# Performance work log

Hardware: AMD Instinct MI355X
Metric: run time of the kernel (lower is better)

The kernel has to match this reference:

```python
import jax, jax.numpy as jnp
import numpy as np

LP = 512   # paragraph length (sequential steps)
LQ = 512   # question/context length attended over
B = 24     # batch_size global in source
IN = 150   # in_size (encoder output dim)
H = 150    # self.hidden_size = 2*75


def setup_inputs() -> dict:
    key = jax.random.key(0)
    ks = jax.random.split(key, 12)
    sc = 1.0 / np.sqrt(2 * IN)  # keep pre-activations in a sane range
    return {
        "up": jax.random.normal(ks[0], (LP, B, IN), jnp.float32),
        "uq": jax.random.normal(ks[1], (LQ, B, IN), jnp.float32),
        "v0": jax.random.normal(ks[2], (B, H), jnp.float32),
        "V": jax.random.normal(ks[3], (B, H, 1), jnp.float32),
        "Wp": jax.random.normal(ks[4], (H, 2 * IN), jnp.float32) * sc,
        "Wq": jax.random.normal(ks[5], (H, 2 * IN), jnp.float32) * sc,
        "Wv": jax.random.normal(ks[6], (H, H), jnp.float32) * sc,
        "Wg": jax.random.normal(ks[7], (4 * IN, 4 * IN), jnp.float32) * sc,
        "w_ih": jax.random.normal(ks[8], (3 * H, 2 * IN), jnp.float32) * sc,
        "w_hh": jax.random.normal(ks[9], (3 * H, H), jnp.float32) * sc,
        "b_ih": jnp.zeros((3 * H,), jnp.float32),
        "b_hh": jnp.zeros((3 * H,), jnp.float32),
    }


def _gru_cell(x, h, w_ih, w_hh, b_ih, b_hh):
    # torch.nn.GRUCell semantics
    gi = x @ w_ih.T + b_ih            # [B, 3H]
    gh = h @ w_hh.T + b_hh            # [B, 3H]
    i_r, i_z, i_n = jnp.split(gi, 3, axis=1)
    h_r, h_z, h_n = jnp.split(gh, 3, axis=1)
    r = jax.nn.sigmoid(i_r + h_r)
    z = jax.nn.sigmoid(i_z + h_z)
    n = jnp.tanh(i_n + r * h_n)
    return (1.0 - z) * n + z * h


def reference(up, uq, v0, V, Wp, Wq, Wv, Wg, w_ih, w_hh, b_ih, b_hh):
    in_size = up.shape[-1]
    # mixer = arange -> up[mixer] == up, so concat duplicates features
    Up = jnp.concatenate([up, up], axis=-1)   # [lp, B, 2*in]
    Uq = jnp.concatenate([uq, uq], axis=-1)   # [lq, B, 2*in]
    WUq = jnp.einsum('lbd,hd->lbh', Uq, Wq)   # loop-invariant Wq(Uq), [lq,B,H]
    Uq_b = Uq.transpose(1, 0, 2)              # [B, lq, 2*in]
    Vv = V[:, :, 0]                            # [B, H]

    def step(v, Up_i):                         # Up_i: [B, 2*in]
        Wup = Up_i @ Wp.T                      # [B, H]
        Wvv = v @ Wv.T                         # [B, H]
        x = jnp.tanh(WUq + Wup[None] + Wvv[None])      # [lq, B, H]
        s = jnp.einsum('lbh,bh->bl', x, Vv)            # [B, lq]
        a = jax.nn.softmax(s, axis=1)                  # [B, lq]
        c = jnp.einsum('bl,bld->bd', a, Uq_b)          # [B, 2*in]
        r = jnp.concatenate([Up_i, c], axis=1)         # [B, 4*in]
        g = jax.nn.sigmoid(r @ Wg.T)                   # [B, 4*in]
        c_ = (g * r)[:, 2 * in_size:]                  # gated attended vector
        v_new = _gru_cell(c_, v, w_ih, w_hh, b_ih, b_hh)
        return v_new, v_new

    _, vs = jax.lax.scan(step, v0, Up)  # [lp, B, H]
    # nn.Dropout in eval mode = identity
    return vs
```

## Files before the change

kernel.cpp:

```cpp
#include <hip/hip_runtime.h>
#include <hip/hip_fp16.h>

typedef _Float16 h2 __attribute__((ext_vector_type(2)));

#define OFF_EW     0u
#define OFF_UQT    983040u
#define OFF_WAV    1904640u
#define OFF_WGC    1952640u
#define OFF_WIH    1976640u
#define OFF_WQST   2048640u
#define OFF_WPC    2071140u
#define OFF_WGU    2093940u
#define OFF_UPA    2139540u
#define OFF_GU     3982740u
#define OFF_FLAG   7669140u
#define OFF_EXG    7669156u
#define OFF_XFLG   7709092u
#define WS_FLOATS  7709476u

__device__ __forceinline__ float fast_rcp(float x) { return __builtin_amdgcn_rcpf(x); }
__device__ __forceinline__ float fast_tanh(float x) {
  return 1.f - 2.f * fast_rcp(__expf(2.f * x) + 1.f);
}
__device__ __forceinline__ float fast_sigmoid(float x) {
  return fast_rcp(1.f + __expf(-x));
}

#if defined(__has_builtin)
#if __has_builtin(__builtin_amdgcn_fdot2)
#define HAVE_FDOT2 1
#endif
#if __has_builtin(__builtin_amdgcn_s_setprio)
#define HAVE_SETPRIO 1
#endif
#endif

__device__ __forceinline__ float fdot2(h2 a, h2 b, float c) {
#ifdef HAVE_FDOT2
  return __builtin_amdgcn_fdot2(a, b, c, false);
#else
  return c + (float)a[0] * (float)b[0] + (float)a[1] * (float)b[1];
#endif
}

__device__ __forceinline__ void ast(float* p, float v) {
  __hip_atomic_store(p, v, __ATOMIC_RELAXED, __HIP_MEMORY_SCOPE_AGENT);
}
__device__ __forceinline__ float ald(const float* p) {
  return __hip_atomic_load(p, __ATOMIC_RELAXED, __HIP_MEMORY_SCOPE_AGENT);
}

__global__ void prep_weights(const float* __restrict__ Wq, const float* __restrict__ Wp,
                             const float* __restrict__ Wv, const float* __restrict__ Wg,
                             const float* __restrict__ w_ih, const float* __restrict__ w_hh,
                             float* __restrict__ ws) {
  float* wqsT = ws + OFF_WQST;
  float* WPC  = ws + OFF_WPC;
  float* WGU  = ws + OFF_WGU;
  _Float16* WAV = (_Float16*)(ws + OFF_WAV);
  _Float16* WGC = (_Float16*)(ws + OFF_WGC);
  _Float16* WIHh = (_Float16*)(ws + OFF_WIH);

  int idx = blockIdx.x * blockDim.x + threadIdx.x;
  int n = gridDim.x * blockDim.x;

  for (int i = idx; i < 150 * 150; i += n) {
    int d = i / 150, h = i - d * 150;
    wqsT[i] = Wq[h * 300 + d] + Wq[h * 300 + d + 150];
  }
  for (int i = idx; i < 600 * 160; i += n) {
    int r = i / 160, h = i - r * 160;
    float v = 0.f;
    if (h < 150) v = (r < 150) ? 2.f * Wv[r * 150 + h] : w_hh[(r - 150) * 150 + h];
    WAV[i] = (_Float16)v;
  }
  for (int i = idx; i < 300 * 160; i += n) {
    int r = i / 160, h = i - r * 160;
    int row = (300 + r) * 600;
    float v = (h < 150) ? Wg[row + 300 + h] + Wg[row + 450 + h] : 0.f;
    WGC[i] = (_Float16)v;
  }
  for (int i = idx; i < 450 * 320; i += n) {
    int r = i / 320, p = i - r * 320;
    float v = (p < 300) ? w_ih[r * 300 + p] : 0.f;
    WIHh[i] = (_Float16)v;
  }
  for (int i = idx; i < 150 * 152; i += n) {
    int h = i / 152, d = i - h * 152;
    WPC[i] = (d < 150) ? 2.f * (Wp[h * 300 + d] + Wp[h * 300 + 150 + d]) : 0.f;
  }
  for (int i = idx; i < 300 * 152; i += n) {
    int r = i / 152, d = i - r * 152;
    int row = (300 + r) * 600;
    WGU[i] = (d < 150) ? Wg[row + d] + Wg[row + 150 + d] : 0.f;
  }
  {
    unsigned* xf = (unsigned*)(ws + OFF_XFLG);
    for (int i = idx; i < 24 * 16; i += n) xf[i] = 0u;
  }
}

__global__ __launch_bounds__(192) void prep_ew(const float* __restrict__ uq, float* __restrict__ ws) {
  const float* wqsT = ws + OFF_WQST;
  _Float16* EW = (_Float16*)(ws + OFF_EW);
  const int l = blockIdx.x, b = blockIdx.y;
  __shared__ float sx[150], sDot[150];
  const int t = threadIdx.x;
  if (t < 150) sx[t] = uq[((size_t)l * 24 + b) * 150 + t];
  __syncthreads();
  if (t < 150) {
    float acc = 0.f;
    for (int d = 0; d < 150; ++d) acc += sx[d] * wqsT[d * 150 + t];
    sDot[t] = acc;
  }
  __syncthreads();
  if (t < 160) {
    float val = 1.f;
    if (t < 150) {
      val = __expf(2.f * sDot[t]);
      val = fminf(fmaxf(val, 1e-7f), 60000.f);
    }
    EW[((size_t)b * 512 + l) * 160 + t] = (_Float16)val;
  }
}

__global__ void prep_uqt(const float* __restrict__ uq, float* __restrict__ ws) {
  _Float16* UQT = (_Float16*)(ws + OFF_UQT);
  int idx = blockIdx.x * blockDim.x + threadIdx.x;
  int n = gridDim.x * blockDim.x;
  for (int m = idx; m < 24 * 150 * 512; m += n) {
    int b = m / (150 * 512);
    int rem = m - b * 150 * 512;
    int r = rem >> 9;
    int l = rem & 511;
    UQT[m] = (_Float16)uq[((size_t)l * 24 + b) * 150 + r];
  }
}

__global__ __launch_bounds__(256) void prep_upagu(const float* __restrict__ up, float* __restrict__ ws) {
  const int b = blockIdx.x;
  const int it = blockIdx.y;
  __shared__ float sUp[64][153];
  for (int m = threadIdx.x; m < 64 * 150; m += 256) {
    int il = m / 150, d = m - il * 150;
    sUp[il][d] = up[(((size_t)(it * 64 + il)) * 24 + b) * 150 + d];
  }
  __syncthreads();
  const float* WGU = ws + OFF_WGU;
  const float* WPC = ws + OFF_WPC;
  float* GU  = ws + OFF_GU  + ((size_t)b * 512 + it * 64) * 300;
  float* UPA = ws + OFF_UPA + ((size_t)b * 512 + it * 64) * 150;
  const int il = threadIdx.x & 63, rl = threadIdx.x >> 6;
  for (int r = rl; r < 450; r += 4) {
    const float* w = (r < 300) ? (WGU + (size_t)r * 152) : (WPC + (size_t)(r - 300) * 152);
    float acc = 0.f;
    for (int d = 0; d < 150; ++d) acc = fmaf(w[d], sUp[il][d], acc);
    if (r < 300) GU[(size_t)il * 300 + r] = acc;
    else         UPA[(size_t)il * 150 + (r - 300)] = acc;
  }
}

__global__ __launch_bounds__(1024) void pq_main(
    const float* __restrict__ v0, const float* __restrict__ Vfull,
    const float* __restrict__ b_ih, const float* __restrict__ b_hh,
    float* __restrict__ ws, float* __restrict__ out) {
  const int blk = blockIdx.x;
  const int x = blk & 7, s = blk >> 3;
  int t3 = -1;
  if (s == 0 || s == 1) t3 = 0;
  else if (s == 10 || s == 11) t3 = 1;
  else if (s == 20 || s == 21) t3 = 2;

  if (t3 < 0) {
    if (threadIdx.x >= 64) return;
    unsigned* flag = (unsigned*)(ws + OFF_FLAG);
    const unsigned long long start = __builtin_amdgcn_s_memrealtime();
    float a0 = 0.f, a1 = 0.f, a2 = 0.f, a3 = 0.f, a4 = 0.f, a5 = 0.f, a6 = 0.f, a7 = 0.f;
    const float m = 1.0000001f, c = 0.9999999f;
    for (;;) {
      #pragma unroll 32
      for (int k = 0; k < 1024; ++k) {
        a0 = fmaf(a0, m, c); a1 = fmaf(a1, m, c); a2 = fmaf(a2, m, c); a3 = fmaf(a3, m, c);
        a4 = fmaf(a4, m, c); a5 = fmaf(a5, m, c); a6 = fmaf(a6, m, c); a7 = fmaf(a7, m, c);
      }
      if (__hip_atomic_load(flag, __ATOMIC_RELAXED, __HIP_MEMORY_SCOPE_AGENT) == 0xDEADBEEFu) break;
      if (__builtin_amdgcn_s_memrealtime() - start > 3000000ull) break;
    }
    float sink = ((a0 + a1) + (a2 + a3)) + ((a4 + a5) + (a6 + a7));
    if (sink == 123.456789f) out[0] = sink;
    return;
  }

#ifdef HAVE_SETPRIO
  __builtin_amdgcn_s_setprio(3);
#endif

  const int hf = s & 1;
  const int b = x + 8 * t3;
  const int tid = threadIdx.x;

  const int EYB = hf ? 80 : 0, EYW = hf ? 70 : 80;
  const int PEYB = hf ? 0 : 80, PEYW = hf ? 80 : 70;
  const int CQB = hf ? 160 : 0, CQW = hf ? 140 : 160;
  const int NA  = 4 * EYW;
  const int NP4 = 3 * EYW;

  const _Float16* EWh  = (const _Float16*)(ws + OFF_EW);
  const _Float16* UQTh = (const _Float16*)(ws + OFF_UQT);
  const _Float16* WAV  = (const _Float16*)(ws + OFF_WAV);
  const _Float16* WIHh = (const _Float16*)(ws + OFF_WIH);
  const float* UPAb = ws + OFF_UPA + (size_t)b * 512 * 150;
  const float* GUb  = ws + OFF_GU  + (size_t)b * 512 * 300;

  float* EX = ws + OFF_EXG + (size_t)b * 1664;
  float* exS0 = EX;
  float* exS1 = EX + 512;
  float* exC  = EX + 1024;
  float* exCQ = EX + 1184;
  float* exV  = EX + 1488;
  float* exSmine = hf ? exS1 : exS0;
  unsigned* FLG = (unsigned*)(ws + OFF_XFLG);
  unsigned* myflag = FLG + (b * 16 + hf * 8);
  unsigned* pflag  = FLG + (b * 16 + (1 - hf) * 8);

  __shared__ float sTmpA[608];
  __shared__ float eyl[160];
  __shared__ float vvl[160];
  __shared__ float sC[152];
  __shared__ float sGip[456];
  __shared__ float sBih[456], sBhh[456];
  __shared__ float sVl[152];
  __shared__ float sRed[8], sRedB[8];
  __shared__ float sSumV;
  __shared__ h2 sAhp2[272];
  __shared__ h2 vop2[80];
  __shared__ h2 ox2[80];
  __shared__ h2 cq2[160];
  __shared__ h2 sWv2[12000];
  __shared__ h2 sWGC2[24000];
  _Float16* sAhx = (_Float16*)sAhp2;
  _Float16* vop = (_Float16*)vop2;
  _Float16* ox  = (_Float16*)ox2;
  _Float16* cq  = (_Float16*)cq2;

  const int g = tid >> 3, j = tid & 7;
  const int g16 = tid >> 4, j16 = tid & 15;

  if (tid < 160) {
    vop[tid] = (_Float16)((tid < 150) ? v0[b * 150 + tid] : 0.f);
    vvl[tid] = (tid < 150) ? Vfull[b * 150 + tid] : 0.f;
    eyl[tid] = 1.f;
  } else if (tid < 320) {
    ox[tid - 160] = (_Float16)0.f;
  } else if (tid < 640) {
    cq[tid - 320] = (_Float16)0.f;
  }
  if (tid >= 512 && tid < 968) {
    int p = tid - 512;
    sBih[p] = (p < 450) ? b_ih[p] : 0.f;
    sBhh[p] = (p < 450) ? b_hh[p] : 0.f;
  }
  if (tid < 152) sVl[tid] = (tid < 150) ? v0[b * 150 + tid] : 0.f;
  {
    const unsigned* srcv = (const unsigned*)(ws + OFF_WAV);
    unsigned* dv = (unsigned*)sWv2;
    for (int k = tid; k < 12000; k += 1024) dv[k] = srcv[k];
    const unsigned* srcg = (const unsigned*)(ws + OFF_WGC);
    unsigned* dg = (unsigned*)sWGC2;
    for (int k = tid; k < 24000; k += 1024) dg[k] = srcg[k];
  }
  __syncthreads();
  if (tid >= 192 && tid < 256) {
    int ln = tid - 192;
    float sm = 0.f;
    for (int h = ln; h < 150; h += 64) sm += vvl[h];
    #pragma unroll
    for (int off = 32; off; off >>= 1) sm += __shfl_xor(sm, off, 64);
    if (ln == 0) sSumV = sm;
  }
  __syncthreads();

  #define XSYNC(K)                                                                   \
    __syncthreads();                                                                 \
    if (tid == 0) {                                                                  \
      __hip_atomic_store(myflag + (K), (unsigned)(i + 1), __ATOMIC_RELAXED,          \
                         __HIP_MEMORY_SCOPE_AGENT);                                  \
      const unsigned long long t0 = __builtin_amdgcn_s_memrealtime();                \
      while (__hip_atomic_load(pflag + (K), __ATOMIC_RELAXED,                        \
                               __HIP_MEMORY_SCOPE_AGENT) < (unsigned)(i + 1)) {      \
        __builtin_amdgcn_s_sleep(1);                                                 \
        if (__builtin_amdgcn_s_memrealtime() - t0 > 20000000ull) break;     \
      }                                                                              \
    }                                                                                \
    __syncthreads();

  for (int i = 0; i < 512; ++i) {
    {
      h2 va[10];
      #pragma unroll
      for (int t = 0; t < 10; ++t) va[t] = vop2[j * 10 + t];
      #pragma unroll
      for (int it = 0; it < 3; ++it) {
        const int idx = g + (it << 7);
        if (idx < NA) {
          const int k = (idx >= 3 * EYW) ? 3 : (idx >= 2 * EYW) ? 2 : (idx >= EYW) ? 1 : 0;
          const int o = idx - k * EYW;
          float acc = 0.f;
          if (k == 0) {
            const int row = EYB + o;
            const h2* wp = sWv2 + row * 80 + j * 10;
            h2 w[10];
            #pragma unroll
            for (int t = 0; t < 10; ++t) w[t] = wp[t];
            #pragma unroll
            for (int t = 0; t < 10; ++t) acc = fdot2(w[t], va[t], acc);
            acc += __shfl_xor(acc, 1, 64);
            acc += __shfl_xor(acc, 2, 64);
            acc += __shfl_xor(acc, 4, 64);
            if (j == 0) {
              float ua = UPAb[(size_t)i * 150 + row];
              eyl[row] = fminf(__expf(ua + acc), 1e30f);
            }
          } else {
            const int rt = k * 150 + EYB + o;
            const h2* wp = (const h2*)WAV + (size_t)rt * 80 + j * 10;
            h2 w[10];
            #pragma unroll
            for (int t = 0; t < 10; ++t) w[t] = wp[t];
            #pragma unroll
            for (int t = 0; t < 10; ++t) acc = fdot2(w[t], va[t], acc);
            acc += __shfl_xor(acc, 1, 64);
            acc += __shfl_xor(acc, 2, 64);
            acc += __shfl_xor(acc, 4, 64);
            if (j == 0) sTmpA[rt] = acc;
          }
        }
      }
    }
    __syncthreads();
    {
      float ey[10], vv[10];
      #pragma unroll
      for (int t = 0; t < 10; ++t) {
        ey[t] = eyl[EYB + j * 10 + t];
        vv[t] = vvl[EYB + j * 10 + t];
      }
      #pragma unroll
      for (int it = 0; it < 4; ++it) {
        const int l = g + (it << 7);
        const h2* wp = (const h2*)(EWh + ((size_t)b * 512 + l) * 160) + (EYB >> 1) + j * 5;
        h2 w[5];
        #pragma unroll
        for (int t = 0; t < 5; ++t) w[t] = wp[t];
        float acc = 0.f;
        #pragma unroll
        for (int t = 0; t < 5; ++t) {
          float x1 = fmaf((float)w[t][0], ey[2 * t],     1.f);
          float y1 = fmaf((float)w[t][1], ey[2 * t + 1], 1.f);
          float num = fmaf(vv[2 * t], y1, vv[2 * t + 1] * x1);
          acc = fmaf(num, fast_rcp(x1 * y1), acc);
        }
        acc += __shfl_xor(acc, 1, 64);
        acc += __shfl_xor(acc, 2, 64);
        acc += __shfl_xor(acc, 4, 64);
        if (j == 0) ast(&exSmine[l], acc);
      }
    }
    XSYNC(0)
    {
      const bool act = tid < 512;
      float sv = act ? (sSumV - 2.f * (ald(&exS0[tid]) + ald(&exS1[tid]))) : -3.4e38f;
      float m = sv;
      #pragma unroll
      for (int off = 32; off; off >>= 1) m = fmaxf(m, __shfl_xor(m, off, 64));
      float e = act ? __expf(sv - m) : 0.f;
      float z = e;
      #pragma unroll
      for (int off = 32; off; off >>= 1) z += __shfl_xor(z, off, 64);
      if (act && (tid & 63) == 0) { sRed[tid >> 6] = m; sRedB[tid >> 6] = z; }
      __syncthreads();
      if (act) {
        float M = sRed[0];
        #pragma unroll
        for (int w = 1; w < 8; ++w) M = fmaxf(M, sRed[w]);
        float Z = 0.f;
        #pragma unroll
        for (int w = 0; w < 8; ++w) Z += sRedB[w] * __expf(sRed[w] - M);
        float a = (e * __expf(m - M)) * fast_rcp(Z);
        sAhx[(tid >> 5) * 34 + (tid & 31)] = (_Float16)a;
      }
    }
    __syncthreads();
    {
      h2 aa[16];
      #pragma unroll
      for (int t = 0; t < 16; ++t) aa[t] = sAhp2[j16 * 17 + t];
      #pragma unroll
      for (int it = 0; it < 2; ++it) {
        const int idx = g16 + (it << 6);
        if (idx < EYW) {
          const int r = EYB + idx;
          const h2* wp = (const h2*)(UQTh + ((size_t)b * 150 + r) * 512) + j16 * 16;
          h2 w[16];
          #pragma unroll
          for (int t = 0; t < 16; ++t) w[t] = wp[t];
          float acc = 0.f;
          #pragma unroll
          for (int t = 0; t < 16; ++t) acc = fdot2(aa[t], w[t], acc);
          acc += __shfl_xor(acc, 1, 64);
          acc += __shfl_xor(acc, 2, 64);
          acc += __shfl_xor(acc, 4, 64);
          acc += __shfl_xor(acc, 8, 64);
          if (j16 == 0) ast(&exC[r], acc);
        }
      }
    }
    XSYNC(1)
    if (tid < 152) {
      float f = (tid < 150) ? ald(&exC[tid]) : 0.f;
      sC[tid] = f;
      ox[tid] = (_Float16)f;
    }
    __syncthreads();
    {
      h2 xa[10];
      #pragma unroll
      for (int t = 0; t < 10; ++t) xa[t] = ox2[j * 10 + t];
      #pragma unroll
      for (int it = 0; it < 2; ++it) {
        const int idx = g + (it << 7);
        if (idx < CQW) {
          const int r = CQB + idx;
          const h2* wp = sWGC2 + r * 80 + j * 10;
          h2 w[10];
          #pragma unroll
          for (int t = 0; t < 10; ++t) w[t] = wp[t];
          float acc = 0.f;
          #pragma unroll
          for (int t = 0; t < 10; ++t) acc = fdot2(w[t], xa[t], acc);
          acc += __shfl_xor(acc, 1, 64);
          acc += __shfl_xor(acc, 2, 64);
          acc += __shfl_xor(acc, 4, 64);
          if (j == 0) {
            float gu = GUb[(size_t)i * 300 + r];
            float gg = fast_sigmoid(acc + gu);
            int cj = (r >= 150) ? r - 150 : r;
            ast(&exCQ[r], gg * sC[cj]);
          }
        }
      }
    }
    XSYNC(2)
    if (tid < 300) cq[tid] = (_Float16)ald(&exCQ[tid]);
    __syncthreads();
    {
      h2 xa[20];
      #pragma unroll
      for (int t = 0; t < 20; ++t) xa[t] = cq2[j * 20 + t];
      #pragma unroll
      for (int it = 0; it < 2; ++it) {
        const int idx = g + (it << 7);
        if (idx < NP4) {
          const int k = (idx >= 2 * EYW) ? 2 : (idx >= EYW) ? 1 : 0;
          const int o = idx - k * EYW;
          const int r = k * 150 + EYB + o;
          const h2* wp = (const h2*)WIHh + (size_t)r * 160 + j * 20;
          h2 w[20];
          #pragma unroll
          for (int t = 0; t < 20; ++t) w[t] = wp[t];
          float acc = 0.f;
          #pragma unroll
          for (int t = 0; t < 20; ++t) acc = fdot2(w[t], xa[t], acc);
          acc += __shfl_xor(acc, 1, 64);
          acc += __shfl_xor(acc, 2, 64);
          acc += __shfl_xor(acc, 4, 64);
          if (j == 0) sGip[r] = acc;
        }
      }
    }
    __syncthreads();
    if (tid < EYW) {
      const int h = EYB + tid;
      float gh_r = sTmpA[150 + h] + sBhh[h];
      float gh_z = sTmpA[300 + h] + sBhh[150 + h];
      float gh_n = sTmpA[450 + h] + sBhh[300 + h];
      float rg = fast_sigmoid(sGip[h]       + sBih[h]       + gh_r);
      float zg = fast_sigmoid(sGip[150 + h] + sBih[150 + h] + gh_z);
      float nn = fast_tanh(sGip[300 + h] + sBih[300 + h] + rg * gh_n);
      float vn = (1.f - zg) * nn + zg * sVl[h];
      sVl[h] = vn;
      vop[h] = (_Float16)vn;
      ast(&exV[h], vn);
      out[((size_t)i * 24 + b) * 150 + h] = vn;
    }
    XSYNC(3)
    if (tid < PEYW) {
      const int hp = PEYB + tid;
      vop[hp] = (_Float16)ald(&exV[hp]);
    }
    __syncthreads();
  }

  if (b == 0 && hf == 0 && tid == 0) {
    __hip_atomic_store((unsigned*)(ws + OFF_FLAG), 0xDEADBEEFu,
                       __ATOMIC_RELAXED, __HIP_MEMORY_SCOPE_AGENT);
  }
  #undef XSYNC
}

extern "C" void kernel_launch(void* const* d_in, const int* in_sizes, int n_in,
                              void* d_out, int out_size, void* d_ws, size_t ws_size,
                              hipStream_t stream) {
  const float* up   = (const float*)d_in[0];
  const float* uq   = (const float*)d_in[1];
  const float* v0   = (const float*)d_in[2];
  const float* V    = (const float*)d_in[3];
  const float* Wp   = (const float*)d_in[4];
  const float* Wq   = (const float*)d_in[5];
  const float* Wv   = (const float*)d_in[6];
  const float* Wg   = (const float*)d_in[7];
  const float* w_ih = (const float*)d_in[8];
  const float* w_hh = (const float*)d_in[9];
  const float* b_ih = (const float*)d_in[10];
  const float* b_hh = (const float*)d_in[11];
  float* ws  = (float*)d_ws;
  float* out = (float*)d_out;

  if (ws_size < (size_t)WS_FLOATS * sizeof(float)) return;

  prep_weights<<<256, 256, 0, stream>>>(Wq, Wp, Wv, Wg, w_ih, w_hh, ws);
  prep_uqt<<<512, 256, 0, stream>>>(uq, ws);
  prep_ew<<<dim3(512, 24), 192, 0, stream>>>(uq, ws);
  prep_upagu<<<dim3(24, 8), 256, 0, stream>>>(up, ws);
  pq_main<<<256, 1024, 0, stream>>>(v0, V, b_ih, b_hh, ws, out);
}
```

Before: 6.443 ms.

## Split gate matvec by K-half to drop one cross-block sync per step

```diff
diff --git a/kernel.cpp b/kernel.cpp
--- a/kernel.cpp
+++ b/kernel.cpp
@@ -15,8 +15,8 @@
 #define OFF_GU     3982740u
 #define OFF_FLAG   7669140u
 #define OFF_EXG    7669156u
-#define OFF_XFLG   7709092u
-#define WS_FLOATS  7709476u
+#define OFF_XFLG   7718308u
+#define WS_FLOATS  7718708u
 
 __device__ __forceinline__ float fast_rcp(float x) { return __builtin_amdgcn_rcpf(x); }
 __device__ __forceinline__ float fast_tanh(float x) {
@@ -201,7 +201,7 @@
 
   const int EYB = hf ? 80 : 0, EYW = hf ? 70 : 80;
   const int PEYB = hf ? 0 : 80, PEYW = hf ? 80 : 70;
-  const int CQB = hf ? 160 : 0, CQW = hf ? 140 : 160;
+  const int SOFF2 = EYB >> 1;
   const int NA  = 4 * EYW;
   const int NP4 = 3 * EYW;
 
@@ -212,13 +212,15 @@
   const float* UPAb = ws + OFF_UPA + (size_t)b * 512 * 150;
   const float* GUb  = ws + OFF_GU  + (size_t)b * 512 * 300;
 
-  float* EX = ws + OFF_EXG + (size_t)b * 1664;
+  float* EX = ws + OFF_EXG + (size_t)b * 2048;
   float* exS0 = EX;
   float* exS1 = EX + 512;
   float* exC  = EX + 1024;
-  float* exCQ = EX + 1184;
-  float* exV  = EX + 1488;
+  float* exG0 = EX + 1184;
+  float* exG1 = EX + 1488;
+  float* exV  = EX + 1792;
   float* exSmine = hf ? exS1 : exS0;
+  float* exGmine = hf ? exG1 : exG0;
   unsigned* FLG = (unsigned*)(ws + OFF_XFLG);
   unsigned* myflag = FLG + (b * 16 + hf * 8);
   unsigned* pflag  = FLG + (b * 16 + (1 - hf) * 8);
@@ -226,7 +228,6 @@
   __shared__ float sTmpA[608];
   __shared__ float eyl[160];
   __shared__ float vvl[160];
-  __shared__ float sC[152];
   __shared__ float sGip[456];
   __shared__ float sBih[456], sBhh[456];
   __shared__ float sVl[152];
@@ -348,7 +349,7 @@
       #pragma unroll
       for (int it = 0; it < 4; ++it) {
         const int l = g + (it << 7);
-        const h2* wp = (const h2*)(EWh + ((size_t)b * 512 + l) * 160) + (EYB >> 1) + j * 5;
+        const h2* wp = (const h2*)(EWh + ((size_t)b * 512 + l) * 160) + SOFF2 + j * 5;
         h2 w[5];
         #pragma unroll
         for (int t = 0; t < 5; ++t) w[t] = wp[t];
@@ -411,47 +412,43 @@
           acc += __shfl_xor(acc, 2, 64);
           acc += __shfl_xor(acc, 4, 64);
           acc += __shfl_xor(acc, 8, 64);
-          if (j16 == 0) ast(&exC[r], acc);
+          if (j16 == 0) {
+            ox[r] = (_Float16)acc;
+            ast(&exC[r], acc);
+          }
         }
       }
     }
-    XSYNC(1)
-    if (tid < 152) {
-      float f = (tid < 150) ? ald(&exC[tid]) : 0.f;
-      sC[tid] = f;
-      ox[tid] = (_Float16)f;
-    }
     __syncthreads();
     {
-      h2 xa[10];
-      #pragma unroll
-      for (int t = 0; t < 10; ++t) xa[t] = ox2[j * 10 + t];
-      #pragma unroll
-      for (int it = 0; it < 2; ++it) {
-        const int idx = g + (it << 7);
-        if (idx < CQW) {
-          const int r = CQB + idx;
-          const h2* wp = sWGC2 + r * 80 + j * 10;
-          h2 w[10];
+      h2 xa[5];
+      #pragma unroll
+      for (int t = 0; t < 5; ++t) xa[t] = ox2[SOFF2 + j * 5 + t];
+      #pragma unroll
+      for (int it = 0; it < 3; ++it) {
+        const int r = g + (it << 7);
+        if (r < 300) {
+          const h2* wp = sWGC2 + r * 80 + SOFF2 + j * 5;
+          h2 w[5];
           #pragma unroll
-          for (int t = 0; t < 10; ++t) w[t] = wp[t];
+          for (int t = 0; t < 5; ++t) w[t] = wp[t];
           float acc = 0.f;
           #pragma unroll
-          for (int t = 0; t < 10; ++t) acc = fdot2(w[t], xa[t], acc);
+          for (int t = 0; t < 5; ++t) acc = fdot2(w[t], xa[t], acc);
           acc += __shfl_xor(acc, 1, 64);
           acc += __shfl_xor(acc, 2, 64);
           acc += __shfl_xor(acc, 4, 64);
-          if (j == 0) {
-            float gu = GUb[(size_t)i * 300 + r];
-            float gg = fast_sigmoid(acc + gu);
-            int cj = (r >= 150) ? r - 150 : r;
-            ast(&exCQ[r], gg * sC[cj]);
-          }
+          if (j == 0) ast(&exGmine[r], acc);
         }
       }
     }
-    XSYNC(2)
-    if (tid < 300) cq[tid] = (_Float16)ald(&exCQ[tid]);
+    XSYNC(1)
+    if (tid < 300) {
+      float gl = ald(&exG0[tid]) + ald(&exG1[tid]) + GUb[(size_t)i * 300 + tid];
+      float gg = fast_sigmoid(gl);
+      int cj = (tid >= 150) ? tid - 150 : tid;
+      cq[tid] = (_Float16)(gg * ald(&exC[cj]));
+    }
     __syncthreads();
     {
       h2 xa[20];
@@ -493,7 +490,7 @@
       ast(&exV[h], vn);
       out[((size_t)i * 24 + b) * 150 + h] = vn;
     }
-    XSYNC(3)
+    XSYNC(2)
     if (tid < PEYW) {
       const int hp = PEYB + tid;
       vop[hp] = (_Float16)ald(&exV[hp]);
```

Result: faster. 5.851 ms (-9.2%).
